# Kernel optimization log

Measured on AMD Instinct MI355X. Metric: run time of the kernel, lower is better.

Reference implementation:

```python
import jax, jax.numpy as jnp
import numpy as np

D_MODEL = 1024
D_STATE = 16
EXPAND = 2
D_INNER = EXPAND * D_MODEL
DT_RANK = 64  # ceil(1024/16)
D_CONV = 4


def setup_inputs() -> dict:
    key = jax.random.key(0)
    ks = jax.random.split(key, 8)
    s = 0.02
    x = jax.random.normal(ks[0], (2, 2048, D_MODEL), dtype=jnp.float32)
    W_in = jax.random.normal(ks[1], (D_MODEL, 2 * D_INNER), dtype=jnp.float32) * s
    W_conv = jax.random.normal(ks[2], (D_CONV, D_INNER), dtype=jnp.float32) * s  # depthwise taps
    b_conv = jnp.zeros((D_INNER,), dtype=jnp.float32)
    W_xproj = jax.random.normal(ks[3], (D_INNER, DT_RANK + 2 * D_STATE), dtype=jnp.float32) * s
    W_dt = jax.random.normal(ks[4], (DT_RANK, D_INNER), dtype=jnp.float32) * s
    b_dt = jnp.zeros((D_INNER,), dtype=jnp.float32)
    A_log = jnp.broadcast_to(jnp.log(jnp.arange(1, D_STATE + 1, dtype=jnp.float32)), (D_INNER, D_STATE))
    D = jnp.ones((D_INNER,), dtype=jnp.float32)
    W_out = jax.random.normal(ks[5], (D_INNER, D_MODEL), dtype=jnp.float32) * s
    return {"x": x, "W_in": W_in, "W_conv": W_conv, "b_conv": b_conv,
            "W_xproj": W_xproj, "W_dt": W_dt, "b_dt": b_dt,
            "A_log": A_log, "D": D, "W_out": W_out}


def _silu(v):
    return v * jax.nn.sigmoid(v)


def reference(x, W_in, W_conv, b_conv, W_xproj, W_dt, b_dt, A_log, D, W_out):
    B_, L, _ = x.shape
    xz = x @ W_in                     # [B, L, 2*d_inner]
    x_in, z = jnp.split(xz, 2, axis=-1)
    # causal depthwise conv1d (torch padding=d_conv-1 then slice to seq_len)
    pad = D_CONV - 1
    x_pad = jnp.pad(x_in, ((0, 0), (pad, 0), (0, 0)))
    x_conv = b_conv
    x_conv = sum(x_pad[:, k:k + L, :] * W_conv[k] for k in range(D_CONV)) + b_conv
    x_in = _silu(x_conv)              # [B, L, d_inner]
    dbc = x_in @ W_xproj
    dt = jax.nn.softplus(dbc[..., :DT_RANK] @ W_dt + b_dt)   # [B, L, d_inner]
    Bm = dbc[..., DT_RANK:DT_RANK + D_STATE]                  # [B, L, d_state]
    Cm = dbc[..., DT_RANK + D_STATE:]                          # [B, L, d_state]
    A = -jnp.exp(A_log)                                        # [d_inner, d_state]

    def step(state, inp):
        x_t, dt_t, B_t, C_t = inp   # [B,d_inner], [B,d_inner], [B,d_state], [B,d_state]
        dA = jnp.exp(jnp.clip(dt_t[:, :, None] * A[None], -10.0, 10.0))
        dB = dt_t[:, :, None] * B_t[:, None, :]
        state = jnp.clip(state * dA + x_t[:, :, None] * dB, -10.0, 10.0)
        y_t = jnp.einsum('bdn,bn->bd', state, C_t) + D * x_t
        return state, y_t

    tm = lambda a: jnp.swapaxes(a, 0, 1)  # time-major
    state0 = jnp.zeros((B_, D_INNER, D_STATE), dtype=x.dtype)
    _, ys = jax.lax.scan(step, state0, (tm(x_in), tm(dt), tm(Bm), tm(Cm)))
    y = jnp.swapaxes(ys, 0, 1)            # [B, L, d_inner]
    y = y * _silu(z)
    return y @ W_out                       # [B, L, d_model]
```

## Files before the change

kernel.cpp:

```cpp
#include <hip/hip_runtime.h>
#include <math.h>

#define D_MODEL 1024
#define D_INNER 2048
#define D_STATE 16
#define DT_RANK 64
#define LSEQ 2048
#define NBATCH 2
#define M_TOT (NBATCH * LSEQ)
#define DBC_STRIDE 128
#define CH 64
#define NCH (LSEQ / CH)
#define KSPL 8
#define OKSPL 2

typedef unsigned short ushort_t;
typedef unsigned int uint_t;
typedef __attribute__((ext_vector_type(8))) short bf16x8;
typedef __attribute__((ext_vector_type(4))) float f32x4;

__device__ __forceinline__ ushort_t f2bf_rne(float f) {
    uint_t u = __float_as_uint(f);
    u += 0x7fffu + ((u >> 16) & 1u);
    return (ushort_t)(u >> 16);
}
__device__ __forceinline__ float bf2f(ushort_t h) {
    return __uint_as_float(((uint_t)h) << 16);
}

#define KIN 1024
#define KTI (KIN / 64)

#define BAR()   __builtin_amdgcn_s_barrier()
#define LGKM0() asm volatile("s_waitcnt lgkmcnt(0)" ::: "memory")

#define LDFRAG_B(SRC)                                                          \
    _Pragma("unroll")                                                          \
    for (int nf = 0; nf < 4; ++nf)                                             \
        fB[nf] = *reinterpret_cast<const bf16x8*>(                             \
            &(SRC)[(bRow + nf * 16 + fm) * 32 + swz * 8]);

#define LDFRAG_A(SRC, MOFF)                                                    \
    _Pragma("unroll")                                                          \
    for (int mf = 0; mf < 4; ++mf)                                             \
        fA[mf] = *reinterpret_cast<const bf16x8*>(                             \
            &(SRC)[(aRow + (MOFF + mf) * 16 + fm) * 32 + swz * 8]);

#define MFMA_QUAD(MOFF)                                                        \
    __builtin_amdgcn_s_setprio(1);                                             \
    _Pragma("unroll")                                                          \
    for (int mf = 0; mf < 4; ++mf)                                             \
        _Pragma("unroll")                                                      \
        for (int nf = 0; nf < 4; ++nf)                                         \
            acc[MOFF + mf][nf] = __builtin_amdgcn_mfma_f32_16x16x32_bf16(      \
                fA[mf], fB[nf], acc[MOFF + mf][nf], 0, 0, 0);                  \
    __builtin_amdgcn_s_setprio(0);

__global__ __launch_bounds__(512, 2) void gemm256_inproj(
    const ushort_t* __restrict__ Ah, const ushort_t* __restrict__ BTh,
    float* __restrict__ C, float* __restrict__ AUX)
{
    __shared__ __align__(1024) ushort_t smem[65536];
    const int tid  = threadIdx.x;
    const int lane = tid & 63;
    const int w    = tid >> 6;
    const int wm   = w >> 2;
    const int wn   = w & 3;
    const int fm   = lane & 15, fk = lane >> 4;
    const int swz  = fk ^ ((fm >> 1) & 3);
    const int aRow = wm * 128;
    const int bRow = wn * 64;
    const int m0   = blockIdx.y * 256;
    const int n0   = blockIdx.x * 256;
    const int rbase = w * 16 + (lane >> 2);
    const int ssw   = ((lane & 3) ^ ((lane >> 3) & 3)) * 8;

    f32x4 acc[8][4] = {};

    auto stage = [&](const ushort_t* __restrict__ g, int grow0, int kcol,
                     int regUS) {
        #pragma unroll
        for (int q = 0; q < 2; ++q) {
            const ushort_t* src =
                g + (size_t)(grow0 + q * 128 + rbase) * KIN + kcol + ssw;
            __builtin_amdgcn_global_load_lds(
                (const __attribute__((address_space(1))) void*)src,
                (__attribute__((address_space(3))) void*)(smem + regUS +
                                                          q * 4096 + w * 512),
                16, 0, 0);
        }
    };

    stage(Ah,  m0, 0,  0);
    stage(BTh, n0, 0,  32768);
    stage(Ah,  m0, 32, 8192);
    stage(BTh, n0, 32, 32768 + 8192);
    stage(Ah,  m0, 64, 16384);
    stage(BTh, n0, 64, 32768 + 16384);
    asm volatile("s_waitcnt vmcnt(8)" ::: "memory");
    BAR();

    bf16x8 fA[4], fB[4];

    for (int t = 0; t < KTI - 1; ++t) {
        const int bf = t & 1, bn = bf ^ 1;
        const ushort_t* A0 = smem + (bf * 2 + 0) * 8192;
        const ushort_t* A1 = smem + (bf * 2 + 1) * 8192;
        const ushort_t* B0 = smem + 32768 + (bf * 2 + 0) * 8192;
        const ushort_t* B1 = smem + 32768 + (bf * 2 + 1) * 8192;
        const int kc1 = (t + 1) * 64, kc2 = (t + 2) * 64;
        const bool st2 = (t + 2 < KTI);

        LDFRAG_B(B0);
        LDFRAG_A(A0, 0);
        stage(Ah, m0, kc1 + 32, (bn * 2 + 1) * 8192);
        BAR(); LGKM0();
        MFMA_QUAD(0);
        BAR();

        LDFRAG_A(A0, 4);
        stage(BTh, n0, kc1 + 32, 32768 + (bn * 2 + 1) * 8192);
        BAR(); LGKM0();
        MFMA_QUAD(4);
        asm volatile("s_waitcnt vmcnt(8)" ::: "memory");
        BAR();
        __builtin_amdgcn_sched_barrier(0);

        LDFRAG_B(B1);
        LDFRAG_A(A1, 0);
        if (st2) stage(Ah, m0, kc2, (bf * 2 + 0) * 8192);
        BAR(); LGKM0();
        MFMA_QUAD(0);
        BAR();

        LDFRAG_A(A1, 4);
        if (st2) stage(BTh, n0, kc2, 32768 + (bf * 2 + 0) * 8192);
        BAR(); LGKM0();
        MFMA_QUAD(4);
        if (t == KTI - 2) { asm volatile("s_waitcnt vmcnt(4)" ::: "memory"); }
        else              { asm volatile("s_waitcnt vmcnt(6)" ::: "memory"); }
        BAR();
        __builtin_amdgcn_sched_barrier(0);
    }

    {
        const int bf = (KTI - 1) & 1;
        const ushort_t* A0 = smem + (bf * 2 + 0) * 8192;
        const ushort_t* A1 = smem + (bf * 2 + 1) * 8192;
        const ushort_t* B0 = smem + 32768 + (bf * 2 + 0) * 8192;
        const ushort_t* B1 = smem + 32768 + (bf * 2 + 1) * 8192;

        LDFRAG_B(B0);
        LDFRAG_A(A0, 0);
        BAR(); LGKM0();
        MFMA_QUAD(0);
        BAR();

        LDFRAG_A(A0, 4);
        BAR(); LGKM0();
        MFMA_QUAD(4);
        asm volatile("s_waitcnt vmcnt(0)" ::: "memory");
        BAR();

        LDFRAG_B(B1);
        LDFRAG_A(A1, 0);
        BAR(); LGKM0();
        MFMA_QUAD(0);
        BAR();

        LDFRAG_A(A1, 4);
        BAR(); LGKM0();
        MFMA_QUAD(4);
    }

    if (n0 < D_INNER) {
        #pragma unroll
        for (int mf = 0; mf < 8; ++mf) {
            int row0 = m0 + aRow + mf * 16 + fk * 4;
            #pragma unroll
            for (int nf = 0; nf < 4; ++nf) {
                int col = n0 + bRow + nf * 16 + fm;
                #pragma unroll
                for (int r = 0; r < 4; ++r)
                    C[(size_t)(row0 + r) * D_INNER + col] = acc[mf][nf][r];
            }
        }
    } else {
        #pragma unroll
        for (int mf = 0; mf < 8; ++mf) {
            int row0 = m0 + aRow + mf * 16 + fk * 4;
            #pragma unroll
            for (int nf = 0; nf < 4; ++nf) {
                int col = n0 + bRow + nf * 16 + fm;
                *reinterpret_cast<f32x4*>(
                    &AUX[(size_t)(col - D_INNER) * M_TOT + row0]) = acc[mf][nf];
            }
        }
    }
}

template <int MODE, int TERMS>
__global__ __launch_bounds__(256) void gemm_bf16s(
    const ushort_t* __restrict__ Ah, const ushort_t* __restrict__ Al,
    const ushort_t* __restrict__ BTh, const ushort_t* __restrict__ BTl,
    float* __restrict__ C, float* __restrict__ AUX, int M, int N, int K)
{
    __shared__ __align__(16) ushort_t smem[4 * 128 * 32];
    ushort_t* sAh = smem;
    ushort_t* sAl = smem + 4096;
    ushort_t* sBh = smem + 8192;
    ushort_t* sBl = smem + 12288;
    const int tid = threadIdx.x;
    const int lane = tid & 63;
    const int m0 = blockIdx.y * 128;
    int ks = 0, nblk = blockIdx.x;
    if (MODE == 3) { ks = blockIdx.x; nblk = 0; }
    if (MODE == 4) { ks = blockIdx.x >> 3; nblk = blockIdx.x & 7; }
    const int n0 = nblk * 128;
    const int wave = tid >> 6;
    const int mw = (wave & 1) * 64, nw = (wave >> 1) * 64;
    const int fm = lane & 15, fk = lane >> 4;
    const int swz = fk ^ ((fm >> 1) & 3);

    f32x4 acc[4][4] = {};

    const int r_st0 = tid >> 2, cp0 = tid & 3;
    const int r_st1 = (256 + tid) >> 2, cp1 = tid & 3;
    const int cl0 = cp0 ^ ((r_st0 >> 1) & 3);
    const int cl1 = cp1 ^ ((r_st1 >> 1) & 3);
    const int ldsb0 = (tid & ~63) * 16;
    const int ldsb1 = (256 + (tid & ~63)) * 16;

    const int kbeg = (MODE == 3) ? ks * (K / KSPL)
                   : (MODE == 4) ? ks * (K / OKSPL) : 0;
    const int kend = (MODE == 3) ? kbeg + K / KSPL
                   : (MODE == 4) ? kbeg + K / OKSPL : K;

    for (int k0 = kbeg; k0 < kend; k0 += 32) {
        __syncthreads();
        {
            size_t ga0 = (size_t)(m0 + r_st0) * K + k0 + cl0 * 8;
            size_t ga1 = (size_t)(m0 + r_st1) * K + k0 + cl1 * 8;
            size_t gb0 = (size_t)(n0 + r_st0) * K + k0 + cl0 * 8;
            size_t gb1 = (size_t)(n0 + r_st1) * K + k0 + cl1 * 8;
            __builtin_amdgcn_global_load_lds(
                (const __attribute__((address_space(1))) void*)(Ah + ga0),
                (__attribute__((address_space(3))) void*)((char*)sAh + ldsb0), 16, 0, 0);
            __builtin_amdgcn_global_load_lds(
                (const __attribute__((address_space(1))) void*)(Ah + ga1),
                (__attribute__((address_space(3))) void*)((char*)sAh + ldsb1), 16, 0, 0);
            if (TERMS >= 3) {
                __builtin_amdgcn_global_load_lds(
                    (const __attribute__((address_space(1))) void*)(Al + ga0),
                    (__attribute__((address_space(3))) void*)((char*)sAl + ldsb0), 16, 0, 0);
                __builtin_amdgcn_global_load_lds(
                    (const __attribute__((address_space(1))) void*)(Al + ga1),
                    (__attribute__((address_space(3))) void*)((char*)sAl + ldsb1), 16, 0, 0);
            }
            __builtin_amdgcn_global_load_lds(
                (const __attribute__((address_space(1))) void*)(BTh + gb0),
                (__attribute__((address_space(3))) void*)((char*)sBh + ldsb0), 16, 0, 0);
            __builtin_amdgcn_global_load_lds(
                (const __attribute__((address_space(1))) void*)(BTh + gb1),
                (__attribute__((address_space(3))) void*)((char*)sBh + ldsb1), 16, 0, 0);
            if (TERMS >= 2) {
                __builtin_amdgcn_global_load_lds(
                    (const __attribute__((address_space(1))) void*)(BTl + gb0),
                    (__attribute__((address_space(3))) void*)((char*)sBl + ldsb0), 16, 0, 0);
                __builtin_amdgcn_global_load_lds(
                    (const __attribute__((address_space(1))) void*)(BTl + gb1),
                    (__attribute__((address_space(3))) void*)((char*)sBl + ldsb1), 16, 0, 0);
            }
        }
        __syncthreads();

        bf16x8 fAh[4], fAl[4], fBh[4], fBl[4];
        #pragma unroll
        for (int t = 0; t < 4; ++t) {
            int ra = (mw + t * 16 + fm) * 32 + swz * 8;
            int rb = (nw + t * 16 + fm) * 32 + swz * 8;
            fAh[t] = *reinterpret_cast<const bf16x8*>(&sAh[ra]);
            if (TERMS >= 3) fAl[t] = *reinterpret_cast<const bf16x8*>(&sAl[ra]);
            fBh[t] = *reinterpret_cast<const bf16x8*>(&sBh[rb]);
            if (TERMS >= 2) fBl[t] = *reinterpret_cast<const bf16x8*>(&sBl[rb]);
        }
        #pragma unroll
        for (int i = 0; i < 4; ++i)
            #pragma unroll
            for (int j = 0; j < 4; ++j) {
                acc[i][j] = __builtin_amdgcn_mfma_f32_16x16x32_bf16(fAh[i], fBh[j], acc[i][j], 0, 0, 0);
                if (TERMS >= 3)
                    acc[i][j] = __builtin_amdgcn_mfma_f32_16x16x32_bf16(fAl[i], fBh[j], acc[i][j], 0, 0, 0);
                if (TERMS >= 2)
                    acc[i][j] = __builtin_amdgcn_mfma_f32_16x16x32_bf16(fAh[i], fBl[j], acc[i][j], 0, 0, 0);
            }
    }

    float* Cq = (MODE == 3 || MODE == 4) ? C + (size_t)ks * M * N : C;
    #pragma unroll
    for (int i = 0; i < 4; ++i) {
        int row0 = m0 + mw + i * 16 + fk * 4;
        #pragma unroll
        for (int j = 0; j < 4; ++j) {
            int col = n0 + nw + j * 16 + fm;
            if (MODE == 5) {
                const float* bias = (const float*)AUX;
                float bc_ = bias[col];
                f32x4 v;
                #pragma unroll
                for (int r = 0; r < 4; ++r) {
                    float t = acc[i][j][r] + bc_;
                    v[r] = fmaxf(t, 0.f) + log1pf(__expf(-fabsf(t)));
                }
                *reinterpret_cast<f32x4*>(&C[(size_t)col * M + row0]) = v;
            } else {
                #pragma unroll
                for (int r = 0; r < 4; ++r)
                    Cq[(size_t)(row0 + r) * N + col] = acc[i][j][r];
            }
        }
    }
}

__global__ __launch_bounds__(256) void xproj_red_k(
    const float* __restrict__ dbcp, float* __restrict__ dbc,
    float* __restrict__ BCT, ushort_t* __restrict__ dbch)
{
    int g = blockIdx.x * 256 + threadIdx.x;
    int m = g >> 7, c = g & 127;
    float s = 0.f;
    #pragma unroll
    for (int ks = 0; ks < KSPL; ++ks)
        s += dbcp[(size_t)ks * M_TOT * DBC_STRIDE + g];
    dbc[g] = s;
    if (c < 64)
        dbch[(size_t)m * 64 + c] = f2bf_rne(s);
    else if (c < 96)
        BCT[(size_t)(c - 64) * M_TOT + m] = s;
}

__global__ __launch_bounds__(256) void outred_k(
    const float* __restrict__ p, float* __restrict__ out)
{
    int i4 = (blockIdx.x * 256 + threadIdx.x) * 4;
    f32x4 a = *reinterpret_cast<const f32x4*>(p + i4);
    f32x4 b = *reinterpret_cast<const f32x4*>(p + (size_t)M_TOT * D_MODEL + i4);
    *reinterpret_cast<f32x4*>(out + i4) = a + b;
}

__global__ __launch_bounds__(256) void cast_h_k(
    const float* __restrict__ X, ushort_t* __restrict__ Xh)
{
    int i4 = (blockIdx.x * 256 + threadIdx.x) * 4;
    float4 v = *reinterpret_cast<const float4*>(X + i4);
    ushort2 a = make_ushort2(f2bf_rne(v.x), f2bf_rne(v.y));
    ushort2 b = make_ushort2(f2bf_rne(v.z), f2bf_rne(v.w));
    *reinterpret_cast<ushort2*>(Xh + i4)     = a;
    *reinterpret_cast<ushort2*>(Xh + i4 + 2) = b;
}

__global__ __launch_bounds__(256) void transpose_cast_k(
    const float* __restrict__ W, ushort_t* __restrict__ Th, ushort_t* __restrict__ Tl,
    int K, int N)
{
    __shared__ float tile[32][33];
    int n0 = blockIdx.x * 32, k0 = blockIdx.y * 32;
    int tx = threadIdx.x & 31, ty = threadIdx.x >> 5;
    #pragma unroll
    for (int i = 0; i < 32; i += 8)
        tile[ty + i][tx] = W[(size_t)(k0 + ty + i) * N + n0 + tx];
    __syncthreads();
    #pragma unroll
    for (int i = 0; i < 32; i += 8) {
        float v = tile[tx][ty + i];
        ushort_t h = f2bf_rne(v);
        ushort_t l = f2bf_rne(v - bf2f(h));
        size_t o = (size_t)(n0 + ty + i) * K + k0 + tx;
        Th[o] = h; Tl[o] = l;
    }
}

__global__ __launch_bounds__(256) void transpose_cast_pad_k(
    const float* __restrict__ W, ushort_t* __restrict__ Th, int K, int N)
{
    __shared__ float tile[32][33];
    int n0 = blockIdx.x * 32, k0 = blockIdx.y * 32;
    int tx = threadIdx.x & 31, ty = threadIdx.x >> 5;
    #pragma unroll
    for (int i = 0; i < 32; i += 8)
        tile[ty + i][tx] = (n0 + tx < N) ? W[(size_t)(k0 + ty + i) * N + n0 + tx] : 0.f;
    __syncthreads();
    #pragma unroll
    for (int i = 0; i < 32; i += 8) {
        float v = tile[tx][ty + i];
        size_t o = (size_t)(n0 + ty + i) * K + k0 + tx;
        Th[o] = f2bf_rne(v);
    }
}

__global__ __launch_bounds__(256) void conv_silu_k(
    const float* __restrict__ xbuf, const float* __restrict__ Wc,
    const float* __restrict__ bc, ushort_t* __restrict__ xinh,
    float* __restrict__ xT)
{
    __shared__ float tile[67][64];
    const int c0 = blockIdx.x * 64;
    const int m0 = blockIdx.y * 64;
    const int bstart = m0 & ~(LSEQ - 1);
    const int tid = threadIdx.x;

    for (int e = tid; e < 67 * 64; e += 256) {
        int r = e >> 6, c = e & 63;
        int g = m0 - 3 + r;
        tile[r][c] = (g >= bstart) ? xbuf[(size_t)g * D_INNER + c0 + c] : 0.f;
    }
    __syncthreads();

    const int c_l = tid & 63, mg = tid >> 6;
    const int c = c0 + c_l;
    const float w0 = Wc[c], w1 = Wc[D_INNER + c];
    const float w2 = Wc[2 * D_INNER + c], w3 = Wc[3 * D_INNER + c];
    const float bb = bc[c];
    float xtbuf[16];
    #pragma unroll
    for (int mi = 0; mi < 16; ++mi) {
        int r = mg * 16 + mi;
        float acc = bb + tile[r][c_l] * w0 + tile[r + 1][c_l] * w1
                       + tile[r + 2][c_l] * w2 + tile[r + 3][c_l] * w3;
        float sv = acc / (1.f + __expf(-acc));
        xinh[(size_t)(m0 + r) * D_INNER + c] = f2bf_rne(sv);
        xtbuf[mi] = sv;
    }
    float* xtp = xT + (size_t)c * M_TOT + m0 + mg * 16;
    #pragma unroll
    for (int q = 0; q < 4; ++q)
        *reinterpret_cast<float4*>(xtp + 4 * q) =
            make_float4(xtbuf[4 * q], xtbuf[4 * q + 1], xtbuf[4 * q + 2], xtbuf[4 * q + 3]);
}

__global__ __launch_bounds__(256) void scan_sum_k(
    const float* __restrict__ dtT, const float* __restrict__ xT,
    const float* __restrict__ BCT, const float* __restrict__ A_log,
    float* __restrict__ asumb, float* __restrict__ sendb)
{
    __shared__ float sdt[16][68], sx[16][68], sBs[16][68];
    const int tid = threadIdx.x;
    const int c0 = blockIdx.x << 4;
    const int ck = blockIdx.y;
    const int b  = blockIdx.z;
    const size_t boff = (size_t)b * LSEQ + ck * CH;

    {
        int r = tid >> 4, q = (tid & 15) << 2;
        *reinterpret_cast<float4*>(&sdt[r][q]) =
            *reinterpret_cast<const float4*>(dtT + (size_t)(c0 + r) * M_TOT + boff + q);
        *reinterpret_cast<float4*>(&sx[r][q]) =
            *reinterpret_cast<const float4*>(xT + (size_t)(c0 + r) * M_TOT + boff + q);
        *reinterpret_cast<float4*>(&sBs[r][q]) =
            *reinterpret_cast<const float4*>(BCT + (size_t)r * M_TOT + boff + q);
    }
    __syncthreads();

    const int n = tid & 15, ch = tid >> 4;
    const int d = c0 + ch;
    const float Adn = -__expf(A_log[d * D_STATE + n]);
    float s = 0.f, asum = 0.f;
    #pragma unroll 4
    for (int tq = 0; tq < CH / 4; ++tq) {
        f32x4 dv = *reinterpret_cast<const f32x4*>(&sdt[ch][tq * 4]);
        f32x4 xv = *reinterpret_cast<const f32x4*>(&sx[ch][tq * 4]);
        f32x4 Bv = *reinterpret_cast<const f32x4*>(&sBs[n][tq * 4]);
        #pragma unroll
        for (int j = 0; j < 4; ++j) {
            float a = fminf(fmaxf(dv[j] * Adn, -10.f), 10.f);
            asum += a;
            float e = __expf(a);
            float t = s * e + dv[j] * xv[j] * Bv[j];
            s = fminf(fmaxf(t, -10.f), 10.f);
        }
    }
    size_t idx = (((size_t)(b * NCH + ck) * D_INNER) + d) * D_STATE + n;
    asumb[idx] = asum;
    sendb[idx] = s;
}

__global__ __launch_bounds__(256) void scan_fix_k(
    const float* __restrict__ asumb, const float* __restrict__ sendb,
    float* __restrict__ sinb)
{
    int g = blockIdx.x * 256 + threadIdx.x;
    int n = g & 15, d = (g >> 4) & (D_INNER - 1), b = g >> 15;
    float s = 0.f;
    for (int ck = 0; ck < NCH; ++ck) {
        size_t idx = (((size_t)(b * NCH + ck) * D_INNER) + d) * D_STATE + n;
        sinb[idx] = s;
        float t = s * __expf(asumb[idx]) + sendb[idx];
        s = fminf(fmaxf(t, -10.f), 10.f);
    }
}

__global__ __launch_bounds__(256) void scan_apply_k(
    const float* __restrict__ dtT, const float* __restrict__ xT,
    const float* __restrict__ BCT, const float* __restrict__ zT,
    const float* __restrict__ sinb,
    const float* __restrict__ A_log, const float* __restrict__ Dv,
    ushort_t* __restrict__ Yh)
{
    __shared__ float sdt[16][68], sx[16][68], sBs[16][68], sCs[16][68], sz[16][68];
    __shared__ float ps[4][16 * 68];
    const int tid = threadIdx.x;
    const int c0 = blockIdx.x << 4;
    const int ck = blockIdx.y;
    const int b  = blockIdx.z;
    const size_t boff = (size_t)b * LSEQ + ck * CH;

    {
        int r = tid >> 4, q = (tid & 15) << 2;
        *reinterpret_cast<float4*>(&sdt[r][q]) =
            *reinterpret_cast<const float4*>(dtT + (size_t)(c0 + r) * M_TOT + boff + q);
        *reinterpret_cast<float4*>(&sx[r][q]) =
            *reinterpret_cast<const float4*>(xT + (size_t)(c0 + r) * M_TOT + boff + q);
        *reinterpret_cast<float4*>(&sBs[r][q]) =
            *reinterpret_cast<const float4*>(BCT + (size_t)r * M_TOT + boff + q);
        *reinterpret_cast<float4*>(&sCs[r][q]) =
            *reinterpret_cast<const float4*>(BCT + (size_t)(16 + r) * M_TOT + boff + q);
        *reinterpret_cast<float4*>(&sz[r][q]) =
            *reinterpret_cast<const float4*>(zT + (size_t)(c0 + r) * M_TOT + boff + q);
    }
    __syncthreads();

    const int w = tid >> 6, lane = tid & 63;
    const int n = lane & 15, cl = lane >> 4;
    const int t_r = lane >> 2, cl_r = lane & 3;
    const int chs = w * 4 + cl;
    const int d = c0 + chs;
    const int cho = w * 4 + cl_r;
    const int d_out = c0 + cho;
    const float Adn = -__expf(A_log[d * D_STATE + n]);
    const float DdEff = (n == 0) ? Dv[d] : 0.f;
    float s = sinb[(((size_t)(b * NCH + ck) * D_INNER) + d) * D_STATE + n];

    #pragma unroll
    for (int tg = 0; tg < CH / 16; ++tg) {
        #pragma unroll
        for (int tq = 0; tq < 4; ++tq) {
            int t4 = tg * 16 + tq * 4;
            f32x4 dv = *reinterpret_cast<const f32x4*>(&sdt[chs][t4]);
            f32x4 xv = *reinterpret_cast<const f32x4*>(&sx[chs][t4]);
            f32x4 Bv = *reinterpret_cast<const f32x4*>(&sBs[n][t4]);
            f32x4 Cv = *reinterpret_cast<const f32x4*>(&sCs[n][t4]);
            #pragma unroll
            for (int j = 0; j < 4; ++j) {
                float a = fminf(fmaxf(dv[j] * Adn, -10.f), 10.f);
                float e = __expf(a);
                float t = s * e + dv[j] * xv[j] * Bv[j];
                s = fminf(fmaxf(t, -10.f), 10.f);
                ps[w][(tq * 4 + j) * 68 + cl * 16 + n] = s * Cv[j] + DdEff * xv[j];
            }
        }
        __builtin_amdgcn_wave_barrier();
        {
            const float* pb = &ps[w][t_r * 68 + cl_r * 16];
            f32x4 r0 = *reinterpret_cast<const f32x4*>(pb + 0);
            f32x4 r1 = *reinterpret_cast<const f32x4*>(pb + 4);
            f32x4 r2 = *reinterpret_cast<const f32x4*>(pb + 8);
            f32x4 r3 = *reinterpret_cast<const f32x4*>(pb + 12);
            f32x4 sv4 = (r0 + r1) + (r2 + r3);
            float sum = (sv4[0] + sv4[1]) + (sv4[2] + sv4[3]);
            float zz = sz[cho][tg * 16 + t_r];
            float szg = zz / (1.f + __expf(-zz));
            float val = sum * szg;
            size_t om = (boff + tg * 16 + t_r) * D_INNER + d_out;
            Yh[om] = f2bf_rne(val);
        }
        __builtin_amdgcn_wave_barrier();
    }
}

extern "C" void kernel_launch(void* const* d_in, const int* in_sizes, int n_in,
                              void* d_out, int out_size, void* d_ws, size_t ws_size,
                              hipStream_t stream)
{
    const float* x       = (const float*)d_in[0];
    const float* W_in    = (const float*)d_in[1];
    const float* W_conv  = (const float*)d_in[2];
    const float* b_conv  = (const float*)d_in[3];
    const float* W_xproj = (const float*)d_in[4];
    const float* W_dt    = (const float*)d_in[5];
    const float* b_dt    = (const float*)d_in[6];
    const float* A_log   = (const float*)d_in[7];
    const float* Dv      = (const float*)d_in[8];
    const float* W_out   = (const float*)d_in[9];
    float* out = (float*)d_out;

    float* xbuf = (float*)d_ws;
    float* zT   = xbuf + (size_t)M_TOT * D_INNER;
    float* dbc  = zT + (size_t)D_INNER * M_TOT;
    float* BCT  = dbc + (size_t)M_TOT * DBC_STRIDE;
    ushort_t* xh     = (ushort_t*)(BCT + (size_t)32 * M_TOT);
    ushort_t* xl     = xh + (size_t)M_TOT * D_MODEL;
    ushort_t* WinTh  = xl + (size_t)M_TOT * D_MODEL;
    ushort_t* WinTl  = WinTh + (size_t)2 * D_INNER * D_MODEL;
    ushort_t* WoutTh = WinTl + (size_t)2 * D_INNER * D_MODEL;
    ushort_t* WoutTl = WoutTh + (size_t)D_MODEL * D_INNER;
    ushort_t* WxTh   = WoutTl + (size_t)D_MODEL * D_INNER;
    ushort_t* WxTl   = WxTh + (size_t)DBC_STRIDE * D_INNER;
    ushort_t* xinh   = WxTl + (size_t)DBC_STRIDE * D_INNER;
    ushort_t* xinl   = xinh + (size_t)M_TOT * D_INNER;
    ushort_t* yh     = xinl + (size_t)M_TOT * D_INNER;
    ushort_t* yl     = yh + (size_t)M_TOT * D_INNER;
    ushort_t* WdtTh  = yl + (size_t)M_TOT * D_INNER;
    ushort_t* dbch   = WdtTh + (size_t)D_INNER * DT_RANK;
    float* xT   = (float*)xh;
    float* dtT  = (float*)xinh;
    float* dbcp = (float*)yh;
    float* pout = (float*)xh;
    const size_t NSUM = (size_t)NBATCH * NCH * D_INNER * D_STATE;
    float* asumb = xbuf;
    float* sendb = xbuf + NSUM;
    float* sinb  = xbuf + 2 * NSUM;

    cast_h_k<<<(M_TOT * D_MODEL) / 1024, 256, 0, stream>>>(x, xh);
    transpose_cast_pad_k<<<dim3((2 * D_INNER) / 32, D_MODEL / 32), 256, 0, stream>>>(
        W_in, WinTh, D_MODEL, 2 * D_INNER);
    transpose_cast_k<<<dim3(D_MODEL / 32, D_INNER / 32), 256, 0, stream>>>(
        W_out, WoutTh, WoutTl, D_INNER, D_MODEL);
    transpose_cast_pad_k<<<dim3(DBC_STRIDE / 32, D_INNER / 32), 256, 0, stream>>>(
        W_xproj, WxTh, D_INNER, DT_RANK + 2 * D_STATE);
    transpose_cast_pad_k<<<dim3(D_INNER / 32, DT_RANK / 32), 256, 0, stream>>>(
        W_dt, WdtTh, DT_RANK, D_INNER);

    gemm256_inproj<<<dim3(16, 16), 512, 0, stream>>>(xh, WinTh, xbuf, zT);
    conv_silu_k<<<dim3(D_INNER / 64, M_TOT / 64), 256, 0, stream>>>(
        xbuf, W_conv, b_conv, xinh, xT);
    gemm_bf16s<3, 1><<<dim3(KSPL, 32), 256, 0, stream>>>(
        xinh, nullptr, WxTh, nullptr, dbcp, nullptr, M_TOT, DBC_STRIDE, D_INNER);
    xproj_red_k<<<(M_TOT * DBC_STRIDE) / 256, 256, 0, stream>>>(dbcp, dbc, BCT, dbch);
    gemm_bf16s<5, 1><<<dim3(D_INNER / 128, M_TOT / 128), 256, 0, stream>>>(
        dbch, nullptr, WdtTh, nullptr, dtT, (float*)b_dt, M_TOT, D_INNER, DT_RANK);
    scan_sum_k<<<dim3(D_INNER / 16, NCH, NBATCH), 256, 0, stream>>>(
        dtT, xT, BCT, A_log, asumb, sendb);
    scan_fix_k<<<(NBATCH * D_INNER * D_STATE) / 256, 256, 0, stream>>>(
        asumb, sendb, sinb);
    scan_apply_k<<<dim3(D_INNER / 16, NCH, NBATCH), 256, 0, stream>>>(
        dtT, xT, BCT, zT, sinb, A_log, Dv, yh);
    gemm_bf16s<4, 2><<<dim3(OKSPL * 8, 32), 256, 0, stream>>>(
        yh, nullptr, WoutTh, WoutTl, pout, nullptr, M_TOT, D_MODEL, D_INNER);
    outred_k<<<(M_TOT * D_MODEL) / 1024, 256, 0, stream>>>(pout, out);
}
```

Baseline: 359.2 us.

## Switch scan to row-major layout with one thread per channel holding all states

The in-projection, conv and dt GEMM now write z, x and dt row-major instead of transposed. The scan kernels assign one thread per channel, keep all 16 state values in registers, and stage time rows into LDS with global_load_lds. B and C are read directly from dbc, so the BCT transpose is gone. It also swaps exp/clip for exp2, fmed3 and rcp intrinsics, and removes the cross-lane partial-sum reduction for y. In exchange, blocks per scan shrink from 16 channels to 256 channels, which leaves fewer blocks (8x32x2) and adds register pressure.

```diff
diff --git a/kernel.cpp b/kernel.cpp
--- a/kernel.cpp
+++ b/kernel.cpp
@@ -27,6 +27,30 @@
 __device__ __forceinline__ float bf2f(ushort_t h) {
     return __uint_as_float(((uint_t)h) << 16);
 }
+__device__ __forceinline__ float fexp2(float x) {
+#if __has_builtin(__builtin_amdgcn_exp2f)
+    return __builtin_amdgcn_exp2f(x);
+#else
+    return exp2f(x);
+#endif
+}
+__device__ __forceinline__ float frcp(float x) {
+#if __has_builtin(__builtin_amdgcn_rcpf)
+    return __builtin_amdgcn_rcpf(x);
+#else
+    return 1.f / x;
+#endif
+}
+__device__ __forceinline__ float clip10(float x) {
+#if __has_builtin(__builtin_amdgcn_fmed3f)
+    return __builtin_amdgcn_fmed3f(x, -10.f, 10.f);
+#else
+    return fminf(fmaxf(x, -10.f), 10.f);
+#endif
+}
+
+#define LOG2E 1.44269504f
+#define NLOG2E10 -14.4269504f
 
 #define KIN 1024
 #define KTI (KIN / 64)
@@ -173,28 +197,17 @@
         MFMA_QUAD(4);
     }
 
-    if (n0 < D_INNER) {
+    float* dst = (n0 < D_INNER) ? C : AUX;
+    const int csub = (n0 < D_INNER) ? 0 : D_INNER;
+    #pragma unroll
+    for (int mf = 0; mf < 8; ++mf) {
+        int row0 = m0 + aRow + mf * 16 + fk * 4;
         #pragma unroll
-        for (int mf = 0; mf < 8; ++mf) {
-            int row0 = m0 + aRow + mf * 16 + fk * 4;
+        for (int nf = 0; nf < 4; ++nf) {
+            int col = n0 + bRow + nf * 16 + fm - csub;
             #pragma unroll
-            for (int nf = 0; nf < 4; ++nf) {
-                int col = n0 + bRow + nf * 16 + fm;
-                #pragma unroll
-                for (int r = 0; r < 4; ++r)
-                    C[(size_t)(row0 + r) * D_INNER + col] = acc[mf][nf][r];
-            }
-        }
-    } else {
-        #pragma unroll
-        for (int mf = 0; mf < 8; ++mf) {
-            int row0 = m0 + aRow + mf * 16 + fk * 4;
-            #pragma unroll
-            for (int nf = 0; nf < 4; ++nf) {
-                int col = n0 + bRow + nf * 16 + fm;
-                *reinterpret_cast<f32x4*>(
-                    &AUX[(size_t)(col - D_INNER) * M_TOT + row0]) = acc[mf][nf];
-            }
+            for (int r = 0; r < 4; ++r)
+                dst[(size_t)(row0 + r) * D_INNER + col] = acc[mf][nf][r];
         }
     }
 }
@@ -306,13 +319,12 @@
             if (MODE == 5) {
                 const float* bias = (const float*)AUX;
                 float bc_ = bias[col];
-                f32x4 v;
                 #pragma unroll
                 for (int r = 0; r < 4; ++r) {
                     float t = acc[i][j][r] + bc_;
-                    v[r] = fmaxf(t, 0.f) + log1pf(__expf(-fabsf(t)));
+                    C[(size_t)(row0 + r) * N + col] =
+                        fmaxf(t, 0.f) + log1pf(__expf(-fabsf(t)));
                 }
-                *reinterpret_cast<f32x4*>(&C[(size_t)col * M + row0]) = v;
             } else {
                 #pragma unroll
                 for (int r = 0; r < 4; ++r)
@@ -324,7 +336,7 @@
 
 __global__ __launch_bounds__(256) void xproj_red_k(
     const float* __restrict__ dbcp, float* __restrict__ dbc,
-    float* __restrict__ BCT, ushort_t* __restrict__ dbch)
+    ushort_t* __restrict__ dbch)
 {
     int g = blockIdx.x * 256 + threadIdx.x;
     int m = g >> 7, c = g & 127;
@@ -335,8 +347,6 @@
     dbc[g] = s;
     if (c < 64)
         dbch[(size_t)m * 64 + c] = f2bf_rne(s);
-    else if (c < 96)
-        BCT[(size_t)(c - 64) * M_TOT + m] = s;
 }
 
 __global__ __launch_bounds__(256) void outred_k(
@@ -401,7 +411,7 @@
 __global__ __launch_bounds__(256) void conv_silu_k(
     const float* __restrict__ xbuf, const float* __restrict__ Wc,
     const float* __restrict__ bc, ushort_t* __restrict__ xinh,
-    float* __restrict__ xT)
+    float* __restrict__ xf)
 {
     __shared__ float tile[67][64];
     const int c0 = blockIdx.x * 64;
@@ -421,7 +431,6 @@
     const float w0 = Wc[c], w1 = Wc[D_INNER + c];
     const float w2 = Wc[2 * D_INNER + c], w3 = Wc[3 * D_INNER + c];
     const float bb = bc[c];
-    float xtbuf[16];
     #pragma unroll
     for (int mi = 0; mi < 16; ++mi) {
         int r = mg * 16 + mi;
@@ -429,151 +438,187 @@
                        + tile[r + 2][c_l] * w2 + tile[r + 3][c_l] * w3;
         float sv = acc / (1.f + __expf(-acc));
         xinh[(size_t)(m0 + r) * D_INNER + c] = f2bf_rne(sv);
-        xtbuf[mi] = sv;
-    }
-    float* xtp = xT + (size_t)c * M_TOT + m0 + mg * 16;
-    #pragma unroll
-    for (int q = 0; q < 4; ++q)
-        *reinterpret_cast<float4*>(xtp + 4 * q) =
-            make_float4(xtbuf[4 * q], xtbuf[4 * q + 1], xtbuf[4 * q + 2], xtbuf[4 * q + 3]);
-}
-
-__global__ __launch_bounds__(256) void scan_sum_k(
-    const float* __restrict__ dtT, const float* __restrict__ xT,
-    const float* __restrict__ BCT, const float* __restrict__ A_log,
+        xf[(size_t)(m0 + r) * D_INNER + c] = sv;
+    }
+}
+
+__global__ __launch_bounds__(256) void scan_sum_k2(
+    const float* __restrict__ dtf, const float* __restrict__ xf,
+    const float* __restrict__ dbc, const float* __restrict__ A_log,
     float* __restrict__ asumb, float* __restrict__ sendb)
 {
-    __shared__ float sdt[16][68], sx[16][68], sBs[16][68];
+    __shared__ float sdt[16][256];
+    __shared__ float sx[16][256];
+    __shared__ float sB[16][16];
     const int tid = threadIdx.x;
-    const int c0 = blockIdx.x << 4;
+    const int lane = tid & 63;
+    const int w = tid >> 6;
+    const int c0 = blockIdx.x << 8;
     const int ck = blockIdx.y;
     const int b  = blockIdx.z;
-    const size_t boff = (size_t)b * LSEQ + ck * CH;
-
-    {
-        int r = tid >> 4, q = (tid & 15) << 2;
-        *reinterpret_cast<float4*>(&sdt[r][q]) =
-            *reinterpret_cast<const float4*>(dtT + (size_t)(c0 + r) * M_TOT + boff + q);
-        *reinterpret_cast<float4*>(&sx[r][q]) =
-            *reinterpret_cast<const float4*>(xT + (size_t)(c0 + r) * M_TOT + boff + q);
-        *reinterpret_cast<float4*>(&sBs[r][q]) =
-            *reinterpret_cast<const float4*>(BCT + (size_t)r * M_TOT + boff + q);
-    }
-    __syncthreads();
-
-    const int n = tid & 15, ch = tid >> 4;
-    const int d = c0 + ch;
-    const float Adn = -__expf(A_log[d * D_STATE + n]);
-    float s = 0.f, asum = 0.f;
-    #pragma unroll 4
-    for (int tq = 0; tq < CH / 4; ++tq) {
-        f32x4 dv = *reinterpret_cast<const f32x4*>(&sdt[ch][tq * 4]);
-        f32x4 xv = *reinterpret_cast<const f32x4*>(&sx[ch][tq * 4]);
-        f32x4 Bv = *reinterpret_cast<const f32x4*>(&sBs[n][tq * 4]);
+    const size_t mbase = (size_t)b * LSEQ + (size_t)ck * CH;
+    const int d = c0 + tid;
+
+    float AdnL2[16];
+    #pragma unroll
+    for (int n = 0; n < 16; ++n)
+        AdnL2[n] = -__expf(A_log[d * D_STATE + n]) * LOG2E;
+
+    float s[16] = {};
+    float asum[16] = {};
+
+    for (int tt = 0; tt < CH / 16; ++tt) {
+        const size_t rowm = mbase + tt * 16;
+        __syncthreads();
         #pragma unroll
-        for (int j = 0; j < 4; ++j) {
-            float a = fminf(fmaxf(dv[j] * Adn, -10.f), 10.f);
-            asum += a;
-            float e = __expf(a);
-            float t = s * e + dv[j] * xv[j] * Bv[j];
-            s = fminf(fmaxf(t, -10.f), 10.f);
-        }
-    }
-    size_t idx = (((size_t)(b * NCH + ck) * D_INNER) + d) * D_STATE + n;
-    asumb[idx] = asum;
-    sendb[idx] = s;
-}
-
-__global__ __launch_bounds__(256) void scan_fix_k(
+        for (int p = 0; p < 4; ++p) {
+            const int r = w + p * 4;
+            const size_t g = (rowm + r) * D_INNER + c0 + lane * 4;
+            __builtin_amdgcn_global_load_lds(
+                (const __attribute__((address_space(1))) void*)(dtf + g),
+                (__attribute__((address_space(3))) void*)(&sdt[r][0]), 16, 0, 0);
+            __builtin_amdgcn_global_load_lds(
+                (const __attribute__((address_space(1))) void*)(xf + g),
+                (__attribute__((address_space(3))) void*)(&sx[r][0]), 16, 0, 0);
+        }
+        if (w == 0) {
+            const int r = lane >> 2, c4 = (lane & 3) * 4;
+            __builtin_amdgcn_global_load_lds(
+                (const __attribute__((address_space(1))) void*)(
+                    dbc + (rowm + r) * DBC_STRIDE + 64 + c4),
+                (__attribute__((address_space(3))) void*)(&sB[0][0]), 16, 0, 0);
+        }
+        __syncthreads();
+
+        #pragma unroll 2
+        for (int t = 0; t < 16; ++t) {
+            const float dv = sdt[t][tid];
+            const float xv = sx[t][tid];
+            const float p  = dv * xv;
+            const f32x4 B0 = *reinterpret_cast<const f32x4*>(&sB[t][0]);
+            const f32x4 B1 = *reinterpret_cast<const f32x4*>(&sB[t][4]);
+            const f32x4 B2 = *reinterpret_cast<const f32x4*>(&sB[t][8]);
+            const f32x4 B3 = *reinterpret_cast<const f32x4*>(&sB[t][12]);
+            #pragma unroll
+            for (int n = 0; n < 16; ++n) {
+                const float Bn = (n < 4) ? B0[n] : (n < 8) ? B1[n - 4]
+                               : (n < 12) ? B2[n - 8] : B3[n - 12];
+                float a = fmaxf(dv * AdnL2[n], NLOG2E10);
+                asum[n] += a;
+                float e = fexp2(a);
+                s[n] = clip10(fmaf(s[n], e, p * Bn));
+            }
+        }
+    }
+    #pragma unroll
+    for (int n = 0; n < 16; ++n) {
+        size_t o = (((size_t)(b * NCH + ck) * 16) + n) * D_INNER + d;
+        asumb[o] = asum[n];
+        sendb[o] = s[n];
+    }
+}
+
+__global__ __launch_bounds__(256) void scan_fix_k2(
     const float* __restrict__ asumb, const float* __restrict__ sendb,
     float* __restrict__ sinb)
 {
     int g = blockIdx.x * 256 + threadIdx.x;
-    int n = g & 15, d = (g >> 4) & (D_INNER - 1), b = g >> 15;
+    int d = g & (D_INNER - 1);
+    int n = (g >> 11) & 15;
+    int b = g >> 15;
     float s = 0.f;
     for (int ck = 0; ck < NCH; ++ck) {
-        size_t idx = (((size_t)(b * NCH + ck) * D_INNER) + d) * D_STATE + n;
+        size_t idx = (((size_t)(b * NCH + ck) * 16) + n) * D_INNER + d;
         sinb[idx] = s;
-        float t = s * __expf(asumb[idx]) + sendb[idx];
-        s = fminf(fmaxf(t, -10.f), 10.f);
-    }
-}
-
-__global__ __launch_bounds__(256) void scan_apply_k(
-    const float* __restrict__ dtT, const float* __restrict__ xT,
-    const float* __restrict__ BCT, const float* __restrict__ zT,
-    const float* __restrict__ sinb,
-    const float* __restrict__ A_log, const float* __restrict__ Dv,
-    ushort_t* __restrict__ Yh)
-{
-    __shared__ float sdt[16][68], sx[16][68], sBs[16][68], sCs[16][68], sz[16][68];
-    __shared__ float ps[4][16 * 68];
+        s = clip10(fmaf(s, fexp2(asumb[idx]), sendb[idx]));
+    }
+}
+
+__global__ __launch_bounds__(256) void scan_apply_k2(
+    const float* __restrict__ dtf, const float* __restrict__ xf,
+    const float* __restrict__ dbc, const float* __restrict__ zf,
+    const float* __restrict__ sinb, const float* __restrict__ A_log,
+    const float* __restrict__ Dv, ushort_t* __restrict__ Yh)
+{
+    __shared__ float sdt[16][256];
+    __shared__ float sx[16][256];
+    __shared__ float sz[16][256];
+    __shared__ float sBC[16][32];
     const int tid = threadIdx.x;
-    const int c0 = blockIdx.x << 4;
+    const int lane = tid & 63;
+    const int w = tid >> 6;
+    const int c0 = blockIdx.x << 8;
     const int ck = blockIdx.y;
     const int b  = blockIdx.z;
-    const size_t boff = (size_t)b * LSEQ + ck * CH;
-
-    {
-        int r = tid >> 4, q = (tid & 15) << 2;
-        *reinterpret_cast<float4*>(&sdt[r][q]) =
-            *reinterpret_cast<const float4*>(dtT + (size_t)(c0 + r) * M_TOT + boff + q);
-        *reinterpret_cast<float4*>(&sx[r][q]) =
-            *reinterpret_cast<const float4*>(xT + (size_t)(c0 + r) * M_TOT + boff + q);
-        *reinterpret_cast<float4*>(&sBs[r][q]) =
-            *reinterpret_cast<const float4*>(BCT + (size_t)r * M_TOT + boff + q);
-        *reinterpret_cast<float4*>(&sCs[r][q]) =
-            *reinterpret_cast<const float4*>(BCT + (size_t)(16 + r) * M_TOT + boff + q);
-        *reinterpret_cast<float4*>(&sz[r][q]) =
-            *reinterpret_cast<const float4*>(zT + (size_t)(c0 + r) * M_TOT + boff + q);
-    }
-    __syncthreads();
-
-    const int w = tid >> 6, lane = tid & 63;
-    const int n = lane & 15, cl = lane >> 4;
-    const int t_r = lane >> 2, cl_r = lane & 3;
-    const int chs = w * 4 + cl;
-    const int d = c0 + chs;
-    const int cho = w * 4 + cl_r;
-    const int d_out = c0 + cho;
-    const float Adn = -__expf(A_log[d * D_STATE + n]);
-    const float DdEff = (n == 0) ? Dv[d] : 0.f;
-    float s = sinb[(((size_t)(b * NCH + ck) * D_INNER) + d) * D_STATE + n];
-
-    #pragma unroll
-    for (int tg = 0; tg < CH / 16; ++tg) {
+    const size_t mbase = (size_t)b * LSEQ + (size_t)ck * CH;
+    const int d = c0 + tid;
+
+    float AdnL2[16];
+    #pragma unroll
+    for (int n = 0; n < 16; ++n)
+        AdnL2[n] = -__expf(A_log[d * D_STATE + n]) * LOG2E;
+    const float Dd = Dv[d];
+
+    float s[16];
+    #pragma unroll
+    for (int n = 0; n < 16; ++n)
+        s[n] = sinb[(((size_t)(b * NCH + ck) * 16) + n) * D_INNER + d];
+
+    for (int tt = 0; tt < CH / 16; ++tt) {
+        const size_t rowm = mbase + tt * 16;
+        __syncthreads();
         #pragma unroll
-        for (int tq = 0; tq < 4; ++tq) {
-            int t4 = tg * 16 + tq * 4;
-            f32x4 dv = *reinterpret_cast<const f32x4*>(&sdt[chs][t4]);
-            f32x4 xv = *reinterpret_cast<const f32x4*>(&sx[chs][t4]);
-            f32x4 Bv = *reinterpret_cast<const f32x4*>(&sBs[n][t4]);
-            f32x4 Cv = *reinterpret_cast<const f32x4*>(&sCs[n][t4]);
+        for (int p = 0; p < 4; ++p) {
+            const int r = w + p * 4;
+            const size_t g = (rowm + r) * D_INNER + c0 + lane * 4;
+            __builtin_amdgcn_global_load_lds(
+                (const __attribute__((address_space(1))) void*)(dtf + g),
+                (__attribute__((address_space(3))) void*)(&sdt[r][0]), 16, 0, 0);
+            __builtin_amdgcn_global_load_lds(
+                (const __attribute__((address_space(1))) void*)(xf + g),
+                (__attribute__((address_space(3))) void*)(&sx[r][0]), 16, 0, 0);
+            __builtin_amdgcn_global_load_lds(
+                (const __attribute__((address_space(1))) void*)(zf + g),
+                (__attribute__((address_space(3))) void*)(&sz[r][0]), 16, 0, 0);
+        }
+        if (w < 2) {
+            const int r = tid >> 3, c8 = (tid & 7) * 4;
+            __builtin_amdgcn_global_load_lds(
+                (const __attribute__((address_space(1))) void*)(
+                    dbc + (rowm + r) * DBC_STRIDE + 64 + c8),
+                (__attribute__((address_space(3))) void*)(&sBC[w * 8][0]), 16, 0, 0);
+        }
+        __syncthreads();
+
+        #pragma unroll 2
+        for (int t = 0; t < 16; ++t) {
+            const float dv = sdt[t][tid];
+            const float xv = sx[t][tid];
+            const float p  = dv * xv;
+            const f32x4 B0 = *reinterpret_cast<const f32x4*>(&sBC[t][0]);
+            const f32x4 B1 = *reinterpret_cast<const f32x4*>(&sBC[t][4]);
+            const f32x4 B2 = *reinterpret_cast<const f32x4*>(&sBC[t][8]);
+            const f32x4 B3 = *reinterpret_cast<const f32x4*>(&sBC[t][12]);
+            const f32x4 C0 = *reinterpret_cast<const f32x4*>(&sBC[t][16]);
+            const f32x4 C1 = *reinterpret_cast<const f32x4*>(&sBC[t][20]);
+            const f32x4 C2 = *reinterpret_cast<const f32x4*>(&sBC[t][24]);
+            const f32x4 C3 = *reinterpret_cast<const f32x4*>(&sBC[t][28]);
+            float y = Dd * xv;
             #pragma unroll
-            for (int j = 0; j < 4; ++j) {
-                float a = fminf(fmaxf(dv[j] * Adn, -10.f), 10.f);
-                float e = __expf(a);
-                float t = s * e + dv[j] * xv[j] * Bv[j];
-                s = fminf(fmaxf(t, -10.f), 10.f);
-                ps[w][(tq * 4 + j) * 68 + cl * 16 + n] = s * Cv[j] + DdEff * xv[j];
+            for (int n = 0; n < 16; ++n) {
+                const float Bn = (n < 4) ? B0[n] : (n < 8) ? B1[n - 4]
+                               : (n < 12) ? B2[n - 8] : B3[n - 12];
+                const float Cn = (n < 4) ? C0[n] : (n < 8) ? C1[n - 4]
+                               : (n < 12) ? C2[n - 8] : C3[n - 12];
+                float a = fmaxf(dv * AdnL2[n], NLOG2E10);
+                float e = fexp2(a);
+                s[n] = clip10(fmaf(s[n], e, p * Bn));
+                y = fmaf(s[n], Cn, y);
             }
-        }
-        __builtin_amdgcn_wave_barrier();
-        {
-            const float* pb = &ps[w][t_r * 68 + cl_r * 16];
-            f32x4 r0 = *reinterpret_cast<const f32x4*>(pb + 0);
-            f32x4 r1 = *reinterpret_cast<const f32x4*>(pb + 4);
-            f32x4 r2 = *reinterpret_cast<const f32x4*>(pb + 8);
-            f32x4 r3 = *reinterpret_cast<const f32x4*>(pb + 12);
-            f32x4 sv4 = (r0 + r1) + (r2 + r3);
-            float sum = (sv4[0] + sv4[1]) + (sv4[2] + sv4[3]);
-            float zz = sz[cho][tg * 16 + t_r];
-            float szg = zz / (1.f + __expf(-zz));
-            float val = sum * szg;
-            size_t om = (boff + tg * 16 + t_r) * D_INNER + d_out;
-            Yh[om] = f2bf_rne(val);
-        }
-        __builtin_amdgcn_wave_barrier();
+            const float zz = sz[t][tid];
+            const float gate = zz * frcp(1.f + fexp2(zz * -LOG2E));
+            Yh[(rowm + t) * D_INNER + d] = f2bf_rne(y * gate);
+        }
     }
 }
 
@@ -594,8 +639,8 @@
     float* out = (float*)d_out;
 
     float* xbuf = (float*)d_ws;
-    float* zT   = xbuf + (size_t)M_TOT * D_INNER;
-    float* dbc  = zT + (size_t)D_INNER * M_TOT;
+    float* zf   = xbuf + (size_t)M_TOT * D_INNER;
+    float* dbc  = zf + (size_t)M_TOT * D_INNER;
     float* BCT  = dbc + (size_t)M_TOT * DBC_STRIDE;
     ushort_t* xh     = (ushort_t*)(BCT + (size_t)32 * M_TOT);
     ushort_t* xl     = xh + (size_t)M_TOT * D_MODEL;
@@ -611,8 +656,8 @@
     ushort_t* yl     = yh + (size_t)M_TOT * D_INNER;
     ushort_t* WdtTh  = yl + (size_t)M_TOT * D_INNER;
     ushort_t* dbch   = WdtTh + (size_t)D_INNER * DT_RANK;
-    float* xT   = (float*)xh;
-    float* dtT  = (float*)xinh;
+    float* xf   = (float*)xh;
+    float* dtf  = (float*)xinh;
     float* dbcp = (float*)yh;
     float* pout = (float*)xh;
     const size_t NSUM = (size_t)NBATCH * NCH * D_INNER * D_STATE;
@@ -630,20 +675,20 @@
     transpose_cast_pad_k<<<dim3(D_INNER / 32, DT_RANK / 32), 256, 0, stream>>>(
         W_dt, WdtTh, DT_RANK, D_INNER);
 
-    gemm256_inproj<<<dim3(16, 16), 512, 0, stream>>>(xh, WinTh, xbuf, zT);
+    gemm256_inproj<<<dim3(16, 16), 512, 0, stream>>>(xh, WinTh, xbuf, zf);
     conv_silu_k<<<dim3(D_INNER / 64, M_TOT / 64), 256, 0, stream>>>(
-        xbuf, W_conv, b_conv, xinh, xT);
+        xbuf, W_conv, b_conv, xinh, xf);
     gemm_bf16s<3, 1><<<dim3(KSPL, 32), 256, 0, stream>>>(
         xinh, nullptr, WxTh, nullptr, dbcp, nullptr, M_TOT, DBC_STRIDE, D_INNER);
-    xproj_red_k<<<(M_TOT * DBC_STRIDE) / 256, 256, 0, stream>>>(dbcp, dbc, BCT, dbch);
+    xproj_red_k<<<(M_TOT * DBC_STRIDE) / 256, 256, 0, stream>>>(dbcp, dbc, dbch);
     gemm_bf16s<5, 1><<<dim3(D_INNER / 128, M_TOT / 128), 256, 0, stream>>>(
-        dbch, nullptr, WdtTh, nullptr, dtT, (float*)b_dt, M_TOT, D_INNER, DT_RANK);
-    scan_sum_k<<<dim3(D_INNER / 16, NCH, NBATCH), 256, 0, stream>>>(
-        dtT, xT, BCT, A_log, asumb, sendb);
-    scan_fix_k<<<(NBATCH * D_INNER * D_STATE) / 256, 256, 0, stream>>>(
+        dbch, nullptr, WdtTh, nullptr, dtf, (float*)b_dt, M_TOT, D_INNER, DT_RANK);
+    scan_sum_k2<<<dim3(D_INNER / 256, NCH, NBATCH), 256, 0, stream>>>(
+        dtf, xf, dbc, A_log, asumb, sendb);
+    scan_fix_k2<<<(NBATCH * D_STATE * D_INNER) / 256, 256, 0, stream>>>(
         asumb, sendb, sinb);
-    scan_apply_k<<<dim3(D_INNER / 16, NCH, NBATCH), 256, 0, stream>>>(
-        dtT, xT, BCT, zT, sinb, A_log, Dv, yh);
+    scan_apply_k2<<<dim3(D_INNER / 256, NCH, NBATCH), 256, 0, stream>>>(
+        dtf, xf, dbc, zf, sinb, A_log, Dv, yh);
     gemm_bf16s<4, 2><<<dim3(OKSPL * 8, 32), 256, 0, stream>>>(
         yh, nullptr, WoutTh, WoutTl, pout, nullptr, M_TOT, D_MODEL, D_INNER);
     outred_k<<<(M_TOT * D_MODEL) / 1024, 256, 0, stream>>>(pout, out);
```

After: 347.3 us. -3.3%, faster.
